# Kernel optimization log

Measured on AMD Instinct MI355X. Metric: run time of the kernel, lower is better.

Reference implementation:

```python
import jax, jax.numpy as jnp
import numpy as np

B, S, H = 2, 8192, 1024
NUM_HEADS = 16
HEAD_DIM = H // NUM_HEADS
KERNEL = 7
DILATION = 1
SCALE = 1.0 / np.sqrt(HEAD_DIM)


def setup_inputs() -> dict:
    key = jax.random.key(0)
    ks = jax.random.split(key, 9)
    init = 0.02
    return {
        "hidden_states": jax.random.normal(ks[0], (B, S, H), dtype=jnp.float32),
        "w_q": jax.random.normal(ks[1], (H, H), dtype=jnp.float32) * init,
        "b_q": jnp.zeros((H,), dtype=jnp.float32),
        "w_k": jax.random.normal(ks[2], (H, H), dtype=jnp.float32) * init,
        "b_k": jnp.zeros((H,), dtype=jnp.float32),
        "w_v": jax.random.normal(ks[3], (H, H), dtype=jnp.float32) * init,
        "b_v": jnp.zeros((H,), dtype=jnp.float32),
        "w_o": jax.random.normal(ks[4], (H, H), dtype=jnp.float32) * init,
        "b_o": jnp.zeros((H,), dtype=jnp.float32),
    }


def reference(hidden_states, w_q, b_q, w_k, b_k, w_v, b_v, w_o, b_o):
    b, s, h = hidden_states.shape
    # QKV projections (weights stored [in, out])
    q = hidden_states @ w_q + b_q
    k = hidden_states @ w_k + b_k
    v = hidden_states @ w_v + b_v
    # [B, nH, S, hd]
    q = q.reshape(b, s, NUM_HEADS, HEAD_DIM).transpose(0, 2, 1, 3)
    k = k.reshape(b, s, NUM_HEADS, HEAD_DIM).transpose(0, 2, 1, 3)
    v = v.reshape(b, s, NUM_HEADS, HEAD_DIM).transpose(0, 2, 1, 3)

    # Neighborhood window indices: for query i, keys at i + (j - K//2)*dilation
    offsets = (jnp.arange(KERNEL) - KERNEL // 2) * DILATION  # [K]
    idx = jnp.arange(s)[:, None] + offsets[None, :]          # [S, K]
    valid = (idx >= 0) & (idx < s)                           # [S, K]
    idx_c = jnp.clip(idx, 0, s - 1)

    k_win = k[:, :, idx_c, :]  # [B, nH, S, K, hd]
    v_win = v[:, :, idx_c, :]  # [B, nH, S, K, hd]

    scores = jnp.einsum('bhsd,bhskd->bhsk', q, k_win) * SCALE
    scores = jnp.where(valid[None, None], scores, -jnp.inf)
    attn = jax.nn.softmax(scores, axis=-1)                   # [B, nH, S, K]
    out = jnp.einsum('bhsk,bhskd->bhsd', attn, v_win)        # [B, nH, S, hd]

    out = out.transpose(0, 2, 1, 3).reshape(b, s, h)
    return out @ w_o + b_o
```

## Files before the change

### kernel.cpp

```cpp
#include <hip/hip_runtime.h>


typedef __bf16 bf16x8 __attribute__((ext_vector_type(8)));
typedef float f32x4 __attribute__((ext_vector_type(4)));
typedef int int4v __attribute__((ext_vector_type(4)));
typedef __attribute__((address_space(1))) void as1_void;
typedef __attribute__((address_space(3))) void as3_void;

__device__ __forceinline__ float bf2f(unsigned short u) {
    union { unsigned int u; float f; } c;
    c.u = ((unsigned int)u) << 16;
    return c.f;
}
__device__ __forceinline__ unsigned short f2bf(float f) {
    union { float f; unsigned int u; } c;
    c.f = f;
    unsigned int u = c.u;
    u += 0x7fffu + ((u >> 16) & 1u);
    return (unsigned short)(u >> 16);
}

__global__ __launch_bounds__(256) void cast_kernel(
    const float* __restrict__ in, unsigned short* __restrict__ out, int n4) {
    int i = blockIdx.x * 256 + threadIdx.x;
    if (i < n4) {
        float4 v = ((const float4*)in)[i];
        ushort4 o;
        o.x = f2bf(v.x); o.y = f2bf(v.y); o.z = f2bf(v.z); o.w = f2bf(v.w);
        ((ushort4*)out)[i] = o;
    }
}

__global__ __launch_bounds__(256) void transpose_cast4(
    const float* __restrict__ w0, const float* __restrict__ w1,
    const float* __restrict__ w2, const float* __restrict__ w3,
    unsigned short* __restrict__ t0, unsigned short* __restrict__ t3) {
    __shared__ unsigned short tile[32][33];
    const int z = blockIdx.z;
    const float* W = (z == 0) ? w0 : (z == 1) ? w1 : (z == 2) ? w2 : w3;
    unsigned short* Wt = (z == 3) ? t3 : t0 + (size_t)z * 1048576;
    const int c0 = blockIdx.x * 32;
    const int r0 = blockIdx.y * 32;
    const int tx = threadIdx.x & 31;
    const int ty = threadIdx.x >> 5;
#pragma unroll
    for (int i = 0; i < 32; i += 8)
        tile[ty + i][tx] = f2bf(W[(size_t)(r0 + ty + i) * 1024 + c0 + tx]);
    __syncthreads();
#pragma unroll
    for (int i = 0; i < 32; i += 8)
        Wt[(size_t)(c0 + ty + i) * 1024 + r0 + tx] = tile[tx][ty + i];
}

__global__ __launch_bounds__(256) void concat_bias(
    const float* __restrict__ a, const float* __restrict__ b,
    const float* __restrict__ c, float* __restrict__ o) {
    int i = blockIdx.x * 256 + threadIdx.x;
    if (i < 3072)
        o[i] = (i < 1024) ? a[i] : ((i < 2048) ? b[i - 1024] : c[i - 2048]);
}

template <int MODE>
__device__ __forceinline__ void gemm_body(
    const unsigned short* __restrict__ A, const unsigned short* __restrict__ Bt,
    const float* __restrict__ bias, float* __restrict__ Cf,
    unsigned short* __restrict__ Cb, unsigned short* __restrict__ Vt,
    int N, int K) {
    __shared__ unsigned short smem[16384];
    const int tid = threadIdx.x;
    const int lane = tid & 63;
    const int wave = tid >> 6;

    const int nbx = gridDim.x;
    const int n = blockIdx.y * nbx + blockIdx.x;
    const int per = nbx * 16;
    const int g = n / per;
    const int rm = n - g * per;
    const int bm = (g * 16 + (rm & 15)) * 128;
    const int bn = (rm >> 4) * 128;

    const int wm = (wave >> 1) * 64;
    const int wn = (wave & 1) * 64;
    const int quad = lane >> 4;
    const int mr = lane & 15;

    const unsigned short* gA[4];
    const unsigned short* gB[4];
    char* lA[4];
    char* lB[4];
#pragma unroll
    for (int k = 0; k < 4; ++k) {
        const int q = (k * 4 + wave) * 64 + lane;
        const int row = q >> 3;
        const int c8 = (q & 7) ^ (row & 7);
        gA[k] = A + (size_t)(bm + row) * K + c8 * 8;
        gB[k] = Bt + (size_t)(bn + row) * K + c8 * 8;
        lA[k] = (char*)smem + (size_t)(k * 4 + wave) * 1024;
        lB[k] = (char*)smem + 16384 + (size_t)(k * 4 + wave) * 1024;
    }

    f32x4 acc[4][4] = {};

    for (int kt = 0; kt < K; kt += 64) {
#pragma unroll
        for (int k = 0; k < 4; ++k) {
            __builtin_amdgcn_global_load_lds((as1_void*)gA[k], (as3_void*)lA[k], 16, 0, 0);
            __builtin_amdgcn_global_load_lds((as1_void*)gB[k], (as3_void*)lB[k], 16, 0, 0);
            gA[k] += 64; gB[k] += 64;
        }
        __syncthreads();

#pragma unroll
        for (int kk = 0; kk < 2; ++kk) {
            bf16x8 af[4], bfr[4];
#pragma unroll
            for (int i = 0; i < 4; ++i) {
                const int R = wm + i * 16 + mr;
                const int c8 = (kk * 4 + quad) ^ (mr & 7);
                af[i] = *(const bf16x8*)(smem + R * 64 + c8 * 8);
            }
#pragma unroll
            for (int j = 0; j < 4; ++j) {
                const int R = wn + j * 16 + mr;
                const int c8 = (kk * 4 + quad) ^ (mr & 7);
                bfr[j] = *(const bf16x8*)(smem + 8192 + R * 64 + c8 * 8);
            }
#pragma unroll
            for (int i = 0; i < 4; ++i)
#pragma unroll
                for (int j = 0; j < 4; ++j)
                    acc[i][j] = __builtin_amdgcn_mfma_f32_16x16x32_bf16(
                        af[i], bfr[j], acc[i][j], 0, 0, 0);
        }
        __syncthreads();
    }

    if (MODE == 0) {
        float* epf = (float*)smem + wave * 2048;
#pragma unroll
        for (int j = 0; j < 4; ++j) {
            const int gcol0 = bn + wn + j * 16;
            const float bv = bias[gcol0 + mr];
#pragma unroll
            for (int i = 0; i < 4; ++i)
#pragma unroll
                for (int r = 0; r < 4; ++r)
                    epf[(i * 16 + quad * 4 + r) * 20 + mr] = acc[i][j][r] + bv;
#pragma unroll
            for (int p = 0; p < 4; ++p) {
                const int dr = p * 16 + (lane >> 2);
                const int ch = lane & 3;
                f32x4 v = *(const f32x4*)(epf + dr * 20 + ch * 4);
                *(f32x4*)(Cf + (size_t)(bm + wm + dr) * N + gcol0 + ch * 4) = v;
            }
        }
    } else if (bn < 2048) {
        unsigned short* epb = smem + wave * 4096;
#pragma unroll
        for (int j = 0; j < 4; ++j) {
            const int gcol0 = bn + wn + j * 16;
            const float bv = bias[gcol0 + mr];
#pragma unroll
            for (int i = 0; i < 4; ++i)
#pragma unroll
                for (int r = 0; r < 4; ++r)
                    epb[(i * 16 + quad * 4 + r) * 20 + mr] = f2bf(acc[i][j][r] + bv);
#pragma unroll
            for (int p = 0; p < 2; ++p) {
                const int dr = p * 32 + (lane >> 1);
                const int ch = lane & 1;
                int4v v = *(const int4v*)(epb + dr * 20 + ch * 8);
                *(int4v*)(Cb + (size_t)(bm + wm + dr) * 2048 + gcol0 + ch * 8) = v;
            }
        }
    } else {
        unsigned short* ep = smem + wave * 4096;
        const int bb = (bm + wm) >> 13;
        const int ssb = (bm + wm) & 8191;
#pragma unroll
        for (int j = 0; j < 4; ++j) {
            const int gcol = bn + wn + j * 16 + mr;
            const float bv = bias[gcol];
#pragma unroll
            for (int i = 0; i < 4; ++i)
#pragma unroll
                for (int r = 0; r < 4; ++r)
                    ep[mr * 68 + i * 16 + quad * 4 + r] = f2bf(acc[i][j][r] + bv);
            const size_t vrow0 = (size_t)(bb * 1024 + (bn - 2048) + wn + j * 16);
#pragma unroll
            for (int p = 0; p < 4; ++p) {
                const int dr = (p * 64 + lane) >> 4;
                const int ch = lane & 15;
                uint2 val = *(const uint2*)(ep + dr * 68 + ch * 4);
                *(uint2*)(Vt + (vrow0 + dr) * 8192 + ssb + ch * 4) = val;
            }
        }
    }
}

__global__ __launch_bounds__(256) void gemm_qkv(
    const unsigned short* __restrict__ A, const unsigned short* __restrict__ Bt,
    const float* __restrict__ bias, unsigned short* __restrict__ Cb,
    unsigned short* __restrict__ Vt, int N, int K) {
    gemm_body<1>(A, Bt, bias, nullptr, Cb, Vt, N, K);
}

__global__ __launch_bounds__(256) void gemm_out(
    const unsigned short* __restrict__ A, const unsigned short* __restrict__ Bt,
    const float* __restrict__ bias, float* __restrict__ Cf, int N, int K) {
    gemm_body<0>(A, Bt, bias, Cf, nullptr, nullptr, N, K);
}

__global__ __launch_bounds__(256) void attn_mfma(
    const unsigned short* __restrict__ QK, const unsigned short* __restrict__ Vt,
    unsigned short* __restrict__ out) {
    __shared__ unsigned short sP[4][64 * 104];
    const int tid = threadIdx.x;
    const int lane = tid & 63;
    const int wave = tid >> 6;
    const int quad = lane >> 4;
    const int cc = lane & 15;
    const int w = blockIdx.x * 4 + wave;
    const int b = w >> 11;
    const int h = (w >> 7) & 15;
    const int st = w & 127;
    const int s0 = st << 6;
    const int win0 = s0 - 8;
    const size_t tokBase = (size_t)b * 8192;
    unsigned short* P = sP[wave];

    {
        int4v z = {0, 0, 0, 0};
#pragma unroll
        for (int i = 0; i < 13; ++i)
            *(int4v*)(P + i * 512 + lane * 8) = z;
    }

    f32x4 accS[4][5] = {};
#pragma unroll
    for (int kc = 0; kc < 2; ++kc) {
        bf16x8 qf[4], kf[5];
#pragma unroll
        for (int mt = 0; mt < 4; ++mt)
            qf[mt] = *(const bf16x8*)(QK + (tokBase + s0 + mt * 16 + cc) * 2048
                                      + h * 64 + kc * 32 + quad * 8);
#pragma unroll
        for (int nt = 0; nt < 5; ++nt) {
            int row = win0 + nt * 16 + cc;
            row = row < 0 ? 0 : (row > 8191 ? 8191 : row);
            kf[nt] = *(const bf16x8*)(QK + (tokBase + row) * 2048
                                      + 1024 + h * 64 + kc * 32 + quad * 8);
        }
#pragma unroll
        for (int mt = 0; mt < 4; ++mt)
#pragma unroll
            for (int nt = 0; nt < 5; ++nt)
                accS[mt][nt] = __builtin_amdgcn_mfma_f32_16x16x32_bf16(
                    qf[mt], kf[nt], accS[mt][nt], 0, 0, 0);
    }

    const float NEG = -__builtin_inff();
#pragma unroll
    for (int mt = 0; mt < 4; ++mt) {
#pragma unroll
        for (int r = 0; r < 4; ++r) {
            const int mrow = mt * 16 + quad * 4 + r;
            float v[5];
#pragma unroll
            for (int nt = 0; nt < 5; ++nt) {
                const int k = nt * 16 + cc;
                const int rel = k - mrow;
                const int sidx = win0 + k;
                const bool ok = (rel >= 5) & (rel <= 11) & (sidx >= 0) & (sidx < 8192);
                v[nt] = ok ? accS[mt][nt][r] * 0.125f : NEG;
            }
            float mx = v[0];
#pragma unroll
            for (int nt = 1; nt < 5; ++nt) mx = fmaxf(mx, v[nt]);
#pragma unroll
            for (int off = 8; off >= 1; off >>= 1) mx = fmaxf(mx, __shfl_xor(mx, off));
            float p[5], sum = 0.f;
#pragma unroll
            for (int nt = 0; nt < 5; ++nt) {
                p[nt] = __builtin_amdgcn_exp2f((v[nt] - mx) * 1.44269504f);
                sum += p[nt];
            }
#pragma unroll
            for (int off = 8; off >= 1; off >>= 1) sum += __shfl_xor(sum, off);
            const float inv = __builtin_amdgcn_rcpf(sum);
#pragma unroll
            for (int nt = 0; nt < 5; ++nt)
                P[mrow * 104 + nt * 16 + cc] = f2bf(p[nt] * inv);
        }
    }

    f32x4 accO[4][4] = {};
#pragma unroll
    for (int kc = 0; kc < 3; ++kc) {
        bf16x8 pf[4], vf[4];
#pragma unroll
        for (int mt = 0; mt < 4; ++mt)
            pf[mt] = *(const bf16x8*)(P + (mt * 16 + cc) * 104 + kc * 32 + quad * 8);
        {
            int pos = win0 + kc * 32 + quad * 8;
            pos = pos < 0 ? 0 : (pos > 8184 ? 8184 : pos);
#pragma unroll
            for (int nt = 0; nt < 4; ++nt)
                vf[nt] = *(const bf16x8*)(Vt + ((size_t)(b * 16 + h) * 64 + nt * 16 + cc) * 8192 + pos);
        }
#pragma unroll
        for (int mt = 0; mt < 4; ++mt)
#pragma unroll
            for (int nt = 0; nt < 4; ++nt)
                accO[mt][nt] = __builtin_amdgcn_mfma_f32_16x16x32_bf16(
                    pf[mt], vf[nt], accO[mt][nt], 0, 0, 0);
    }

#pragma unroll
    for (int mt = 0; mt < 4; ++mt)
#pragma unroll
        for (int nt = 0; nt < 4; ++nt)
#pragma unroll
            for (int r = 0; r < 4; ++r)
                P[(mt * 16 + quad * 4 + r) * 72 + nt * 16 + cc] = f2bf(accO[mt][nt][r]);

#pragma unroll
    for (int pass = 0; pass < 8; ++pass) {
        const int row = pass * 8 + (lane >> 3);
        const int ch = lane & 7;
        int4v vv = *(const int4v*)(P + row * 72 + ch * 8);
        *(int4v*)(out + (tokBase + s0 + row) * 1024 + h * 64 + ch * 8) = vv;
    }
}

extern "C" void kernel_launch(void* const* d_in, const int* in_sizes, int n_in,
                              void* d_out, int out_size, void* d_ws, size_t ws_size,
                              hipStream_t stream) {
    (void)in_sizes; (void)n_in; (void)out_size; (void)ws_size;
    const float* X  = (const float*)d_in[0];
    const float* wq = (const float*)d_in[1];
    const float* bq = (const float*)d_in[2];
    const float* wk = (const float*)d_in[3];
    const float* bk = (const float*)d_in[4];
    const float* wv = (const float*)d_in[5];
    const float* bv = (const float*)d_in[6];
    const float* wo = (const float*)d_in[7];
    const float* bo = (const float*)d_in[8];
    float* out = (float*)d_out;

    char* ws = (char*)d_ws;
    unsigned short* Xb    = (unsigned short*)(ws);
    unsigned short* WtQKV = (unsigned short*)(ws + 33554432);
    unsigned short* WtO   = (unsigned short*)(ws + 39845888);
    unsigned short* QK    = (unsigned short*)(ws + 41943040);
    unsigned short* Vt    = (unsigned short*)(ws + 109051904);
    unsigned short* AttnO = (unsigned short*)(ws + 142606336);
    float*          biasQ = (float*)(ws + 176160768);

    cast_kernel<<<16384, 256, 0, stream>>>(X, Xb, 4194304);
    transpose_cast4<<<dim3(32, 32, 4), 256, 0, stream>>>(wq, wk, wv, wo, WtQKV, WtO);
    concat_bias<<<12, 256, 0, stream>>>(bq, bk, bv, biasQ);

    gemm_qkv<<<dim3(24, 128), 256, 0, stream>>>(Xb, WtQKV, biasQ, QK, Vt, 3072, 1024);

    attn_mfma<<<1024, 256, 0, stream>>>(QK, Vt, AttnO);

    gemm_out<<<dim3(8, 128), 256, 0, stream>>>(AttnO, WtO, bo, out, 1024, 1024);
}
```

Baseline: 354.6 us.

## Enlarge GEMM block tile to 256x128 with 8x4 MFMA accumulators per wave

The shared GEMM body now uses 256-row block tiles, so each wave computes a 128x64 sub-tile with 8x4 accumulators. This halves the number of blocks and reloads of B per unit of output, raising MFMA work per shared-memory load. The grouped block-index swizzle that improved L2 locality is dropped in favour of plain blockIdx mapping. The epilogues are adapted, and the V-transpose store now writes 16-byte chunks. Costs are more registers and LDS per block (launch_bounds asks for 2 blocks per CU), fewer blocks for the out GEMM (512), and possibly worse L2 reuse without the swizzle.

```diff
diff --git a/kernel.cpp b/kernel.cpp
--- a/kernel.cpp
+++ b/kernel.cpp
@@ -66,67 +66,65 @@
     const float* __restrict__ bias, float* __restrict__ Cf,
     unsigned short* __restrict__ Cb, unsigned short* __restrict__ Vt,
     int N, int K) {
-    __shared__ unsigned short smem[16384];
+    __shared__ unsigned short smem[24576];
     const int tid = threadIdx.x;
     const int lane = tid & 63;
     const int wave = tid >> 6;
-
-    const int nbx = gridDim.x;
-    const int n = blockIdx.y * nbx + blockIdx.x;
-    const int per = nbx * 16;
-    const int g = n / per;
-    const int rm = n - g * per;
-    const int bm = (g * 16 + (rm & 15)) * 128;
-    const int bn = (rm >> 4) * 128;
-
-    const int wm = (wave >> 1) * 64;
+    const int bm = blockIdx.y * 256;
+    const int bn = blockIdx.x * 128;
+    const int wm = (wave >> 1) * 128;
     const int wn = (wave & 1) * 64;
     const int quad = lane >> 4;
     const int mr = lane & 15;
 
-    const unsigned short* gA[4];
+    const unsigned short* gA[8];
     const unsigned short* gB[4];
-    char* lA[4];
+    char* lA[8];
     char* lB[4];
+#pragma unroll
+    for (int k = 0; k < 8; ++k) {
+        const int q = (k * 4 + wave) * 64 + lane;
+        const int row = q >> 3;
+        const int c8 = (q & 7) ^ (row & 7);
+        gA[k] = A + (size_t)(bm + row) * K + c8 * 8;
+        lA[k] = (char*)smem + (size_t)(k * 4 + wave) * 1024;
+    }
 #pragma unroll
     for (int k = 0; k < 4; ++k) {
         const int q = (k * 4 + wave) * 64 + lane;
         const int row = q >> 3;
         const int c8 = (q & 7) ^ (row & 7);
-        gA[k] = A + (size_t)(bm + row) * K + c8 * 8;
         gB[k] = Bt + (size_t)(bn + row) * K + c8 * 8;
-        lA[k] = (char*)smem + (size_t)(k * 4 + wave) * 1024;
-        lB[k] = (char*)smem + 16384 + (size_t)(k * 4 + wave) * 1024;
-    }
-
-    f32x4 acc[4][4] = {};
+        lB[k] = (char*)smem + 32768 + (size_t)(k * 4 + wave) * 1024;
+    }
+
+    f32x4 acc[8][4] = {};
 
     for (int kt = 0; kt < K; kt += 64) {
 #pragma unroll
+        for (int k = 0; k < 8; ++k) {
+            __builtin_amdgcn_global_load_lds((as1_void*)gA[k], (as3_void*)lA[k], 16, 0, 0);
+            gA[k] += 64;
+        }
+#pragma unroll
         for (int k = 0; k < 4; ++k) {
-            __builtin_amdgcn_global_load_lds((as1_void*)gA[k], (as3_void*)lA[k], 16, 0, 0);
             __builtin_amdgcn_global_load_lds((as1_void*)gB[k], (as3_void*)lB[k], 16, 0, 0);
-            gA[k] += 64; gB[k] += 64;
+            gB[k] += 64;
         }
         __syncthreads();
 
 #pragma unroll
         for (int kk = 0; kk < 2; ++kk) {
-            bf16x8 af[4], bfr[4];
-#pragma unroll
-            for (int i = 0; i < 4; ++i) {
-                const int R = wm + i * 16 + mr;
-                const int c8 = (kk * 4 + quad) ^ (mr & 7);
-                af[i] = *(const bf16x8*)(smem + R * 64 + c8 * 8);
-            }
-#pragma unroll
-            for (int j = 0; j < 4; ++j) {
-                const int R = wn + j * 16 + mr;
-                const int c8 = (kk * 4 + quad) ^ (mr & 7);
-                bfr[j] = *(const bf16x8*)(smem + 8192 + R * 64 + c8 * 8);
-            }
-#pragma unroll
-            for (int i = 0; i < 4; ++i)
+            const int c8 = (kk * 4 + quad) ^ (mr & 7);
+            bf16x8 af[8], bfr[4];
+#pragma unroll
+            for (int i = 0; i < 8; ++i)
+                af[i] = *(const bf16x8*)(smem + (wm + i * 16 + mr) * 64 + c8 * 8);
+#pragma unroll
+            for (int j = 0; j < 4; ++j)
+                bfr[j] = *(const bf16x8*)(smem + 16384 + (wn + j * 16 + mr) * 64 + c8 * 8);
+#pragma unroll
+            for (int i = 0; i < 8; ++i)
 #pragma unroll
                 for (int j = 0; j < 4; ++j)
                     acc[i][j] = __builtin_amdgcn_mfma_f32_16x16x32_bf16(
@@ -135,46 +133,48 @@
         __syncthreads();
     }
 
+    unsigned short* ep = smem + wave * 4096;
     if (MODE == 0) {
-        float* epf = (float*)smem + wave * 2048;
+        float* epf = (float*)ep;
 #pragma unroll
         for (int j = 0; j < 4; ++j) {
             const int gcol0 = bn + wn + j * 16;
             const float bv = bias[gcol0 + mr];
 #pragma unroll
-            for (int i = 0; i < 4; ++i)
-#pragma unroll
-                for (int r = 0; r < 4; ++r)
-                    epf[(i * 16 + quad * 4 + r) * 20 + mr] = acc[i][j][r] + bv;
-#pragma unroll
-            for (int p = 0; p < 4; ++p) {
-                const int dr = p * 16 + (lane >> 2);
-                const int ch = lane & 3;
-                f32x4 v = *(const f32x4*)(epf + dr * 20 + ch * 4);
-                *(f32x4*)(Cf + (size_t)(bm + wm + dr) * N + gcol0 + ch * 4) = v;
+            for (int h2 = 0; h2 < 2; ++h2) {
+#pragma unroll
+                for (int i2 = 0; i2 < 4; ++i2)
+#pragma unroll
+                    for (int r = 0; r < 4; ++r)
+                        epf[(i2 * 16 + quad * 4 + r) * 20 + mr] = acc[h2 * 4 + i2][j][r] + bv;
+#pragma unroll
+                for (int p = 0; p < 4; ++p) {
+                    const int dr = p * 16 + (lane >> 2);
+                    const int ch = lane & 3;
+                    f32x4 v = *(const f32x4*)(epf + dr * 20 + ch * 4);
+                    *(f32x4*)(Cf + (size_t)(bm + wm + h2 * 64 + dr) * N + gcol0 + ch * 4) = v;
+                }
             }
         }
     } else if (bn < 2048) {
-        unsigned short* epb = smem + wave * 4096;
 #pragma unroll
         for (int j = 0; j < 4; ++j) {
             const int gcol0 = bn + wn + j * 16;
             const float bv = bias[gcol0 + mr];
 #pragma unroll
-            for (int i = 0; i < 4; ++i)
+            for (int i = 0; i < 8; ++i)
 #pragma unroll
                 for (int r = 0; r < 4; ++r)
-                    epb[(i * 16 + quad * 4 + r) * 20 + mr] = f2bf(acc[i][j][r] + bv);
-#pragma unroll
-            for (int p = 0; p < 2; ++p) {
+                    ep[(i * 16 + quad * 4 + r) * 20 + mr] = f2bf(acc[i][j][r] + bv);
+#pragma unroll
+            for (int p = 0; p < 4; ++p) {
                 const int dr = p * 32 + (lane >> 1);
                 const int ch = lane & 1;
-                int4v v = *(const int4v*)(epb + dr * 20 + ch * 8);
+                int4v v = *(const int4v*)(ep + dr * 20 + ch * 8);
                 *(int4v*)(Cb + (size_t)(bm + wm + dr) * 2048 + gcol0 + ch * 8) = v;
             }
         }
     } else {
-        unsigned short* ep = smem + wave * 4096;
         const int bb = (bm + wm) >> 13;
         const int ssb = (bm + wm) & 8191;
 #pragma unroll
@@ -182,30 +182,30 @@
             const int gcol = bn + wn + j * 16 + mr;
             const float bv = bias[gcol];
 #pragma unroll
-            for (int i = 0; i < 4; ++i)
+            for (int i = 0; i < 8; ++i)
 #pragma unroll
                 for (int r = 0; r < 4; ++r)
-                    ep[mr * 68 + i * 16 + quad * 4 + r] = f2bf(acc[i][j][r] + bv);
+                    ep[mr * 132 + i * 16 + quad * 4 + r] = f2bf(acc[i][j][r] + bv);
             const size_t vrow0 = (size_t)(bb * 1024 + (bn - 2048) + wn + j * 16);
 #pragma unroll
             for (int p = 0; p < 4; ++p) {
-                const int dr = (p * 64 + lane) >> 4;
+                const int dr = p * 4 + (lane >> 4);
                 const int ch = lane & 15;
-                uint2 val = *(const uint2*)(ep + dr * 68 + ch * 4);
-                *(uint2*)(Vt + (vrow0 + dr) * 8192 + ssb + ch * 4) = val;
-            }
-        }
-    }
-}
-
-__global__ __launch_bounds__(256) void gemm_qkv(
+                int4v v = *(const int4v*)(ep + dr * 132 + ch * 8);
+                *(int4v*)(Vt + (vrow0 + dr) * 8192 + ssb + ch * 8) = v;
+            }
+        }
+    }
+}
+
+__global__ __launch_bounds__(256, 2) void gemm_qkv(
     const unsigned short* __restrict__ A, const unsigned short* __restrict__ Bt,
     const float* __restrict__ bias, unsigned short* __restrict__ Cb,
     unsigned short* __restrict__ Vt, int N, int K) {
     gemm_body<1>(A, Bt, bias, nullptr, Cb, Vt, N, K);
 }
 
-__global__ __launch_bounds__(256) void gemm_out(
+__global__ __launch_bounds__(256, 2) void gemm_out(
     const unsigned short* __restrict__ A, const unsigned short* __restrict__ Bt,
     const float* __restrict__ bias, float* __restrict__ Cf, int N, int K) {
     gemm_body<0>(A, Bt, bias, Cf, nullptr, nullptr, N, K);
@@ -361,9 +361,9 @@
     transpose_cast4<<<dim3(32, 32, 4), 256, 0, stream>>>(wq, wk, wv, wo, WtQKV, WtO);
     concat_bias<<<12, 256, 0, stream>>>(bq, bk, bv, biasQ);
 
-    gemm_qkv<<<dim3(24, 128), 256, 0, stream>>>(Xb, WtQKV, biasQ, QK, Vt, 3072, 1024);
+    gemm_qkv<<<dim3(24, 64), 256, 0, stream>>>(Xb, WtQKV, biasQ, QK, Vt, 3072, 1024);
 
     attn_mfma<<<1024, 256, 0, stream>>>(QK, Vt, AttnO);
 
-    gemm_out<<<dim3(8, 128), 256, 0, stream>>>(AttnO, WtO, bo, out, 1024, 1024);
-}
+    gemm_out<<<dim3(8, 64), 256, 0, stream>>>(AttnO, WtO, bo, out, 1024, 1024);
+}
```

Result: faster. 341.1 us (-3.8%).
